# Kernel optimization log

Measured on AMD Instinct MI355X. Metric: run time of the kernel, lower is better.

## Reference

```python
import jax, jax.numpy as jnp
import numpy as np

B = 16384          # batch
NS = 26            # sparse features
ND = 13            # dense features
V = 100000         # vocab per sparse feature
E = 16             # embedding size
H = 400            # dnn hidden
DNN_IN = NS * E + ND  # 429


def setup_inputs() -> dict:
    key = jax.random.key(0)
    ks = jax.random.split(key, 12)
    X_sparse = jax.random.randint(ks[0], (B, NS), 0, V, dtype=jnp.int32)
    X_dense = jax.random.normal(ks[1], (B, ND), dtype=jnp.float32)
    # stacked per-feature embedding tables: [NS, V, dim]
    emb1 = jax.random.normal(ks[2], (NS, V, 1), dtype=jnp.float32) * 1e-4
    emb2 = jax.random.normal(ks[3], (NS, V, E), dtype=jnp.float32) * 1e-4
    lin_weight = jax.random.normal(ks[4], (ND, 1), dtype=jnp.float32) * 1e-4
    bias = jnp.zeros((1,), dtype=jnp.float32)
    W0 = jax.random.normal(ks[5], (DNN_IN, H), dtype=jnp.float32) * 1e-4
    b0 = jnp.zeros((H,), dtype=jnp.float32)
    W1 = jax.random.normal(ks[6], (H, H), dtype=jnp.float32) * 1e-4
    b1 = jnp.zeros((H,), dtype=jnp.float32)
    W2 = jax.random.normal(ks[7], (H, H), dtype=jnp.float32) * 1e-4
    b2 = jnp.zeros((H,), dtype=jnp.float32)
    W_out = jax.random.normal(ks[8], (H, 1), dtype=jnp.float32) * 1e-4
    return {"X_sparse": X_sparse, "X_dense": X_dense, "emb1": emb1, "emb2": emb2,
            "lin_weight": lin_weight, "bias": bias, "W0": W0, "b0": b0,
            "W1": W1, "b1": b1, "W2": W2, "b2": b2, "W_out": W_out}


def reference(X_sparse, X_dense, emb1, emb2, lin_weight, bias, W0, b0, W1, b1, W2, b2, W_out):
    fidx = jnp.arange(NS)[None, :]            # [1, NS] feature indices
    # ---- FM linear term ----
    e1 = emb1[fidx, X_sparse][..., 0]          # [B, NS] per-feature scalar embeddings
    linear_sparse = jnp.sum(e1, axis=-1, keepdims=True)            # [B, 1]
    linear_dense = X_dense @ lin_weight                            # [B, 1]
    logit = linear_sparse + linear_dense
    # ---- FM second-order cross term ----
    e2 = emb2[fidx, X_sparse]                  # [B, NS, E]
    square_of_sum = jnp.square(jnp.sum(e2, axis=1))                # [B, E]
    sum_of_square = jnp.sum(jnp.square(e2), axis=1)                # [B, E]
    cross = 0.5 * jnp.sum(square_of_sum - sum_of_square, axis=-1, keepdims=True)
    logit = logit + cross
    # ---- DNN (dropout p=0 -> identity) ----
    dnn_in = jnp.concatenate([e2.reshape(e2.shape[0], -1), X_dense], axis=-1)  # [B, 429]
    h = jax.nn.relu(dnn_in @ W0 + b0)
    h = jax.nn.relu(h @ W1 + b1)
    h = jax.nn.relu(h @ W2 + b2)
    logit = logit + h @ W_out
    return logit + bias
```

## Files before the change

kernel.cpp:

```cpp
#include <hip/hip_runtime.h>
#include <hip/hip_bf16.h>

#define B_     16384
#define NS_    26
#define ND_    13
#define V_     100000
#define E_     16
#define H_     400
#define NP     448
#define K0A    429

typedef __bf16 bf16x8 __attribute__((ext_vector_type(8)));
typedef float  f32x4  __attribute__((ext_vector_type(4)));

__device__ __forceinline__ unsigned short f2bf(float f) {
  __hip_bfloat16 h = __float2bfloat16(f);
  return __builtin_bit_cast(unsigned short, h);
}

__global__ __launch_bounds__(256) void fm_kernel(
    const int* __restrict__ Xs, const float* __restrict__ Xd,
    const float* __restrict__ emb1, const float* __restrict__ emb2,
    const float* __restrict__ linw, const float* __restrict__ bias,
    unsigned short* __restrict__ dnn, float* __restrict__ out) {
  const int row  = blockIdx.x * 16 + (threadIdx.x >> 4);
  const int lane = threadIdx.x & 15;
  const int* xs = Xs + row * NS_;
  unsigned short* drow = dnn + (size_t)row * NP;

  float s_sum = 0.f, s_sq = 0.f;
#pragma unroll
  for (int f = 0; f < NS_; ++f) {
    int idx = xs[f];
    float v = emb2[((size_t)f * V_ + idx) * E_ + lane];
    s_sum += v;
    s_sq  += v * v;
    drow[f * 16 + lane] = f2bf(v);
  }

  float lin = 0.f;
  for (int f = lane; f < NS_; f += 16)
    lin += emb1[(size_t)f * V_ + xs[f]];

  float xdv = 0.f;
  if (lane < ND_) {
    xdv = Xd[row * ND_ + lane];
    lin += xdv * linw[lane];
  }
  drow[416 + lane] = f2bf(lane < ND_ ? xdv : 0.f);
  drow[432 + lane] = 0;

  float r = 0.5f * (s_sum * s_sum - s_sq) + lin;
#pragma unroll
  for (int m = 8; m >= 1; m >>= 1) r += __shfl_xor(r, m, 64);
  if (lane == 0) out[row] = r + bias[0];
}

__global__ __launch_bounds__(256) void conv_all(
    const float* __restrict__ W0, const float* __restrict__ W1,
    const float* __restrict__ W2, const float* __restrict__ b0,
    const float* __restrict__ b1, const float* __restrict__ b2,
    const float* __restrict__ Wout,
    unsigned short* __restrict__ W0t, unsigned short* __restrict__ W1t,
    unsigned short* __restrict__ W2t, float* __restrict__ b0p,
    float* __restrict__ b1p, float* __restrict__ b2p,
    float* __restrict__ woutp) {
  const int WSZ = NP * NP;
  int i = blockIdx.x * 256 + threadIdx.x;
  if (i < 3 * WSZ) {
    int which = i / WSZ;
    int j = i - which * WSZ;
    int k = j / NP, n = j - (j / NP) * NP;
    const float* W = (which == 0) ? W0 : (which == 1) ? W1 : W2;
    unsigned short* Wt = (which == 0) ? W0t : (which == 1) ? W1t : W2t;
    int Kact = (which == 0) ? K0A : H_;
    float v = (k < Kact && n < H_) ? W[k * H_ + n] : 0.f;
    Wt[(size_t)n * NP + k] = f2bf(v);
  } else {
    int j = i - 3 * WSZ;
    if (j < NP)          b0p[j]            = (j < H_) ? b0[j] : 0.f;
    else if (j < 2 * NP) b1p[j - NP]       = (j - NP < H_) ? b1[j - NP] : 0.f;
    else if (j < 3 * NP) b2p[j - 2 * NP]   = (j - 2 * NP < H_) ? b2[j - 2 * NP] : 0.f;
    else if (j < 4 * NP) woutp[j - 3 * NP] = (j - 3 * NP < H_) ? Wout[j - 3 * NP] : 0.f;
  }
}

__global__ __launch_bounds__(256) void gemm_relu(
    const unsigned short* __restrict__ A, const unsigned short* __restrict__ Bt,
    const float* __restrict__ bias, unsigned short* __restrict__ C,
    const float* __restrict__ wout, float* __restrict__ out, int fuse) {
  __shared__ unsigned short As[128][40];
  __shared__ unsigned short Bs[64][40];

  const int tid  = threadIdx.x;
  const int wave = tid >> 6;
  const int lane = tid & 63;
  const int quad = lane >> 4;
  const int l16  = lane & 15;
  const int rowBase = blockIdx.x * 128;
  const int colBase = blockIdx.y * 64;

  const int sr = tid >> 2, sseg = tid & 3;
  const unsigned short* aptr0 = A  + (size_t)(rowBase + sr) * NP + sseg * 8;
  const unsigned short* aptr1 = A  + (size_t)(rowBase + 64 + sr) * NP + sseg * 8;
  const unsigned short* bptr  = Bt + (size_t)(colBase + sr) * NP + sseg * 8;

  f32x4 acc[2][4] = {};

  uint4 a0 = *(const uint4*)(aptr0);
  uint4 a1 = *(const uint4*)(aptr1);
  uint4 bv = *(const uint4*)(bptr);

  const int nK = NP / 32;
  for (int kt = 0; kt < nK; ++kt) {
    __syncthreads();
    *(uint4*)&As[sr][sseg * 8]      = a0;
    *(uint4*)&As[64 + sr][sseg * 8] = a1;
    *(uint4*)&Bs[sr][sseg * 8]      = bv;
    __syncthreads();

    if (kt + 1 < nK) {
      a0 = *(const uint4*)(aptr0 + (kt + 1) * 32);
      a1 = *(const uint4*)(aptr1 + (kt + 1) * 32);
      bv = *(const uint4*)(bptr + (kt + 1) * 32);
    }

    bf16x8 af0 = __builtin_bit_cast(bf16x8, *(const uint4*)&As[wave * 32 + l16][quad * 8]);
    bf16x8 af1 = __builtin_bit_cast(bf16x8, *(const uint4*)&As[wave * 32 + 16 + l16][quad * 8]);
#pragma unroll
    for (int nt = 0; nt < 4; ++nt) {
      bf16x8 bf = __builtin_bit_cast(bf16x8, *(const uint4*)&Bs[nt * 16 + l16][quad * 8]);
      acc[0][nt] = __builtin_amdgcn_mfma_f32_16x16x32_bf16(af0, bf, acc[0][nt], 0, 0, 0);
      acc[1][nt] = __builtin_amdgcn_mfma_f32_16x16x32_bf16(af1, bf, acc[1][nt], 0, 0, 0);
    }
  }

  float wsum[2][4] = {};
#pragma unroll
  for (int mt = 0; mt < 2; ++mt) {
#pragma unroll
    for (int nt = 0; nt < 4; ++nt) {
      int col = colBase + nt * 16 + l16;
      float bz = bias[col];
      float wv = wout[col];
#pragma unroll
      for (int r = 0; r < 4; ++r) {
        float v = acc[mt][nt][r] + bz;
        v = v > 0.f ? v : 0.f;
        if (!fuse) {
          int row = rowBase + wave * 32 + mt * 16 + quad * 4 + r;
          C[(size_t)row * NP + col] = f2bf(v);
        } else {
          wsum[mt][r] += v * wv;
        }
      }
    }
  }

  if (fuse) {
#pragma unroll
    for (int mt = 0; mt < 2; ++mt) {
#pragma unroll
      for (int r = 0; r < 4; ++r) {
        float s = wsum[mt][r];
        s += __shfl_xor(s, 1, 64);
        s += __shfl_xor(s, 2, 64);
        s += __shfl_xor(s, 4, 64);
        s += __shfl_xor(s, 8, 64);
        if (l16 == 0) {
          int row = rowBase + wave * 32 + mt * 16 + quad * 4 + r;
          atomicAdd(out + row, s);
        }
      }
    }
  }
}

extern "C" void kernel_launch(void* const* d_in, const int* in_sizes, int n_in,
                              void* d_out, int out_size, void* d_ws, size_t ws_size,
                              hipStream_t stream) {
  const int*   Xs   = (const int*)d_in[0];
  const float* Xd   = (const float*)d_in[1];
  const float* emb1 = (const float*)d_in[2];
  const float* emb2 = (const float*)d_in[3];
  const float* linw = (const float*)d_in[4];
  const float* bias = (const float*)d_in[5];
  const float* W0   = (const float*)d_in[6];
  const float* b0   = (const float*)d_in[7];
  const float* W1   = (const float*)d_in[8];
  const float* b1   = (const float*)d_in[9];
  const float* W2   = (const float*)d_in[10];
  const float* b2   = (const float*)d_in[11];
  const float* Wout = (const float*)d_in[12];
  float* out = (float*)d_out;

  char* ws = (char*)d_ws;
  const size_t PSZ = (size_t)B_ * NP * 2;
  const size_t WSZ = (size_t)NP * NP * 2;
  unsigned short* P0  = (unsigned short*)(ws);
  unsigned short* P1  = (unsigned short*)(ws + PSZ);
  unsigned short* W0t = (unsigned short*)(ws + 2 * PSZ);
  unsigned short* W1t = (unsigned short*)(ws + 2 * PSZ + WSZ);
  unsigned short* W2t = (unsigned short*)(ws + 2 * PSZ + 2 * WSZ);
  float* b0p   = (float*)(ws + 2 * PSZ + 3 * WSZ);
  float* b1p   = (float*)(ws + 2 * PSZ + 3 * WSZ + 1792);
  float* b2p   = (float*)(ws + 2 * PSZ + 3 * WSZ + 2 * 1792);
  float* woutp = (float*)(ws + 2 * PSZ + 3 * WSZ + 3 * 1792);

  fm_kernel<<<B_ / 16, 256, 0, stream>>>(Xs, Xd, emb1, emb2, linw, bias, P0, out);

  conv_all<<<(3 * NP * NP + 4 * NP) / 256, 256, 0, stream>>>(
      W0, W1, W2, b0, b1, b2, Wout, W0t, W1t, W2t, b0p, b1p, b2p, woutp);

  dim3 grid(B_ / 128, NP / 64);
  gemm_relu<<<grid, 256, 0, stream>>>(P0, W0t, b0p, P1, woutp, out, 0);
  gemm_relu<<<grid, 256, 0, stream>>>(P1, W1t, b1p, P0, woutp, out, 0);
  gemm_relu<<<grid, 256, 0, stream>>>(P0, W2t, b2p, P1, woutp, out, 1);
}
```

Baseline: 297.0 us.

## Fuse three DNN layers into one kernel keeping activations in LDS

Replaces the three separate GEMM launches with one kernel per 64-row tile. The tile's activations stay in shared memory across all three layers, and weight K-chunks are streamed through a double buffer with async global-to-LDS loads. The embedding gather and the weight conversion are merged into a single prep launch, and the conversion indexing is changed to write coalesced. This removes the global round-trips of the intermediate activations and two launches, but it re-streams all weights for every tile and runs at one block per CU because of the large LDS footprint.

```diff
diff --git a/kernel.cpp b/kernel.cpp
--- a/kernel.cpp
+++ b/kernel.cpp
@@ -5,10 +5,13 @@
 #define NS_    26
 #define ND_    13
 #define V_     100000
-#define E_     16
 #define H_     400
 #define NP     448
 #define K0A    429
+#define MT     64
+#define ASTR   456
+#define WCH    (448 * 32)
+#define LDSB   (MT * ASTR * 2 + 2 * WCH * 2)
 
 typedef __bf16 bf16x8 __attribute__((ext_vector_type(8)));
 typedef float  f32x4  __attribute__((ext_vector_type(4)));
@@ -18,158 +21,189 @@
   return __builtin_bit_cast(unsigned short, h);
 }
 
-__global__ __launch_bounds__(256) void fm_kernel(
+__global__ __launch_bounds__(256) void prep_kernel(
     const int* __restrict__ Xs, const float* __restrict__ Xd,
     const float* __restrict__ emb1, const float* __restrict__ emb2,
     const float* __restrict__ linw, const float* __restrict__ bias,
-    unsigned short* __restrict__ dnn, float* __restrict__ out) {
-  const int row  = blockIdx.x * 16 + (threadIdx.x >> 4);
-  const int lane = threadIdx.x & 15;
-  const int* xs = Xs + row * NS_;
-  unsigned short* drow = dnn + (size_t)row * NP;
-
-  float s_sum = 0.f, s_sq = 0.f;
-#pragma unroll
-  for (int f = 0; f < NS_; ++f) {
-    int idx = xs[f];
-    float v = emb2[((size_t)f * V_ + idx) * E_ + lane];
-    s_sum += v;
-    s_sq  += v * v;
-    drow[f * 16 + lane] = f2bf(v);
-  }
-
-  float lin = 0.f;
-  for (int f = lane; f < NS_; f += 16)
-    lin += emb1[(size_t)f * V_ + xs[f]];
-
-  float xdv = 0.f;
-  if (lane < ND_) {
-    xdv = Xd[row * ND_ + lane];
-    lin += xdv * linw[lane];
-  }
-  drow[416 + lane] = f2bf(lane < ND_ ? xdv : 0.f);
-  drow[432 + lane] = 0;
-
-  float r = 0.5f * (s_sum * s_sum - s_sq) + lin;
-#pragma unroll
-  for (int m = 8; m >= 1; m >>= 1) r += __shfl_xor(r, m, 64);
-  if (lane == 0) out[row] = r + bias[0];
-}
-
-__global__ __launch_bounds__(256) void conv_all(
     const float* __restrict__ W0, const float* __restrict__ W1,
     const float* __restrict__ W2, const float* __restrict__ b0,
     const float* __restrict__ b1, const float* __restrict__ b2,
     const float* __restrict__ Wout,
-    unsigned short* __restrict__ W0t, unsigned short* __restrict__ W1t,
-    unsigned short* __restrict__ W2t, float* __restrict__ b0p,
-    float* __restrict__ b1p, float* __restrict__ b2p,
-    float* __restrict__ woutp) {
-  const int WSZ = NP * NP;
-  int i = blockIdx.x * 256 + threadIdx.x;
-  if (i < 3 * WSZ) {
-    int which = i / WSZ;
-    int j = i - which * WSZ;
-    int k = j / NP, n = j - (j / NP) * NP;
-    const float* W = (which == 0) ? W0 : (which == 1) ? W1 : W2;
-    unsigned short* Wt = (which == 0) ? W0t : (which == 1) ? W1t : W2t;
-    int Kact = (which == 0) ? K0A : H_;
-    float v = (k < Kact && n < H_) ? W[k * H_ + n] : 0.f;
-    Wt[(size_t)n * NP + k] = f2bf(v);
+    unsigned short* __restrict__ dnn, unsigned short* __restrict__ W0t,
+    unsigned short* __restrict__ W1t, unsigned short* __restrict__ W2t,
+    float* __restrict__ b0p, float* __restrict__ b1p, float* __restrict__ b2p,
+    float* __restrict__ woutp, float* __restrict__ out) {
+  const int blk = blockIdx.x;
+  if (blk < 1024) {
+    const int row  = blk * 16 + (threadIdx.x >> 4);
+    const int lane = threadIdx.x & 15;
+    const int* xs = Xs + row * NS_;
+    unsigned short* drow = dnn + (size_t)row * NP;
+
+    float s_sum = 0.f, s_sq = 0.f;
+#pragma unroll
+    for (int f = 0; f < NS_; ++f) {
+      int idx = xs[f];
+      float v = emb2[((size_t)f * V_ + idx) * 16 + lane];
+      s_sum += v;
+      s_sq  += v * v;
+      drow[f * 16 + lane] = f2bf(v);
+    }
+    float lin = 0.f;
+    for (int f = lane; f < NS_; f += 16)
+      lin += emb1[(size_t)f * V_ + xs[f]];
+    float xdv = 0.f;
+    if (lane < ND_) {
+      xdv = Xd[row * ND_ + lane];
+      lin += xdv * linw[lane];
+    }
+    drow[416 + lane] = f2bf(lane < ND_ ? xdv : 0.f);
+    drow[432 + lane] = 0;
+
+    float r = 0.5f * (s_sum * s_sum - s_sq) + lin;
+#pragma unroll
+    for (int m = 8; m >= 1; m >>= 1) r += __shfl_xor(r, m, 64);
+    if (lane == 0) out[row] = r + bias[0];
   } else {
-    int j = i - 3 * WSZ;
-    if (j < NP)          b0p[j]            = (j < H_) ? b0[j] : 0.f;
-    else if (j < 2 * NP) b1p[j - NP]       = (j - NP < H_) ? b1[j - NP] : 0.f;
-    else if (j < 3 * NP) b2p[j - 2 * NP]   = (j - 2 * NP < H_) ? b2[j - 2 * NP] : 0.f;
-    else if (j < 4 * NP) woutp[j - 3 * NP] = (j - 3 * NP < H_) ? Wout[j - 3 * NP] : 0.f;
-  }
-}
-
-__global__ __launch_bounds__(256) void gemm_relu(
-    const unsigned short* __restrict__ A, const unsigned short* __restrict__ Bt,
-    const float* __restrict__ bias, unsigned short* __restrict__ C,
-    const float* __restrict__ wout, float* __restrict__ out, int fuse) {
-  __shared__ unsigned short As[128][40];
-  __shared__ unsigned short Bs[64][40];
+    const int WSZ = NP * NP;
+    int i = (blk - 1024) * 256 + threadIdx.x;
+    if (i < 3 * WSZ) {
+      int which = i / WSZ;
+      int j = i - which * WSZ;
+      int n = j / NP, k = j - (j / NP) * NP;
+      const float* W = (which == 0) ? W0 : (which == 1) ? W1 : W2;
+      unsigned short* Wt = (which == 0) ? W0t : (which == 1) ? W1t : W2t;
+      int Kact = (which == 0) ? K0A : H_;
+      float v = (k < Kact && n < H_) ? W[k * H_ + n] : 0.f;
+      Wt[(size_t)n * NP + k] = f2bf(v);
+    } else {
+      int j = i - 3 * WSZ;
+      if (j < NP)          b0p[j]            = (j < H_) ? b0[j] : 0.f;
+      else if (j < 2 * NP) b1p[j - NP]       = (j - NP < H_) ? b1[j - NP] : 0.f;
+      else if (j < 3 * NP) b2p[j - 2 * NP]   = (j - 2 * NP < H_) ? b2[j - 2 * NP] : 0.f;
+      else if (j < 4 * NP) woutp[j - 3 * NP] = (j - 3 * NP < H_) ? Wout[j - 3 * NP] : 0.f;
+    }
+  }
+}
+
+__device__ __forceinline__ void stage_w_chunk(
+    const unsigned short* __restrict__ Wt, int kt, unsigned short* wb,
+    int wave, int lane) {
+#pragma unroll
+  for (int i = 0; i < 7; ++i) {
+    int sbase = i * 256 + wave * 64;
+    int s = sbase + lane;
+    int n = s >> 2, g = s & 3;
+    const unsigned short* gp = Wt + n * NP + kt * 32 + g * 8;
+    unsigned short* lp = wb + (size_t)sbase * 8;
+    __builtin_amdgcn_global_load_lds(
+        (const __attribute__((address_space(1))) unsigned int*)gp,
+        (__attribute__((address_space(3))) unsigned int*)lp, 16, 0, 0);
+  }
+}
+
+__global__ __launch_bounds__(256, 1) void fused_dnn(
+    const unsigned short* __restrict__ dnn,
+    const unsigned short* __restrict__ W0t, const unsigned short* __restrict__ W1t,
+    const unsigned short* __restrict__ W2t,
+    const float* __restrict__ b0p, const float* __restrict__ b1p,
+    const float* __restrict__ b2p, const float* __restrict__ woutp,
+    float* __restrict__ out) {
+  extern __shared__ char smem[];
+  unsigned short* act  = (unsigned short*)smem;
+  unsigned short* wbuf = (unsigned short*)(smem + MT * ASTR * 2);
 
   const int tid  = threadIdx.x;
   const int wave = tid >> 6;
   const int lane = tid & 63;
   const int quad = lane >> 4;
   const int l16  = lane & 15;
-  const int rowBase = blockIdx.x * 128;
-  const int colBase = blockIdx.y * 64;
-
-  const int sr = tid >> 2, sseg = tid & 3;
-  const unsigned short* aptr0 = A  + (size_t)(rowBase + sr) * NP + sseg * 8;
-  const unsigned short* aptr1 = A  + (size_t)(rowBase + 64 + sr) * NP + sseg * 8;
-  const unsigned short* bptr  = Bt + (size_t)(colBase + sr) * NP + sseg * 8;
-
-  f32x4 acc[2][4] = {};
-
-  uint4 a0 = *(const uint4*)(aptr0);
-  uint4 a1 = *(const uint4*)(aptr1);
-  uint4 bv = *(const uint4*)(bptr);
-
-  const int nK = NP / 32;
-  for (int kt = 0; kt < nK; ++kt) {
+  const int r0   = blockIdx.x * MT;
+
+#pragma unroll
+  for (int i = 0; i < 7; ++i) {
+    int s = i * 256 + tid;
+    int row = s / 28, gc = s - (s / 28) * 28;
+    uint4 v = *(const uint4*)(dnn + (size_t)(r0 + row) * NP + gc * 8);
+    *(uint4*)(act + row * ASTR + gc * 8) = v;
+  }
+
+  const unsigned short* Wl[3] = {W0t, W1t, W2t};
+  const float* bl[3] = {b0p, b1p, b2p};
+
+  stage_w_chunk(Wl[0], 0, wbuf, wave, lane);
+
+  for (int layer = 0; layer < 3; ++layer) {
+    const unsigned short* Wt = Wl[layer];
+    f32x4 acc[4][7] = {};
+
+    for (int kt = 0; kt < 14; ++kt) {
+      __syncthreads();
+      if (kt + 1 < 14)
+        stage_w_chunk(Wt, kt + 1, wbuf + ((kt + 1) & 1) * WCH, wave, lane);
+      const unsigned short* wb = wbuf + (kt & 1) * WCH;
+
+      bf16x8 af[4];
+#pragma unroll
+      for (int mt = 0; mt < 4; ++mt)
+        af[mt] = __builtin_bit_cast(
+            bf16x8, *(const uint4*)(act + (mt * 16 + l16) * ASTR + kt * 32 + quad * 8));
+#pragma unroll
+      for (int nt = 0; nt < 7; ++nt) {
+        int n = wave * 112 + nt * 16 + l16;
+        bf16x8 bf = __builtin_bit_cast(bf16x8, *(const uint4*)(wb + n * 32 + quad * 8));
+#pragma unroll
+        for (int mt = 0; mt < 4; ++mt)
+          acc[mt][nt] = __builtin_amdgcn_mfma_f32_16x16x32_bf16(af[mt], bf, acc[mt][nt], 0, 0, 0);
+      }
+    }
+
     __syncthreads();
-    *(uint4*)&As[sr][sseg * 8]      = a0;
-    *(uint4*)&As[64 + sr][sseg * 8] = a1;
-    *(uint4*)&Bs[sr][sseg * 8]      = bv;
-    __syncthreads();
-
-    if (kt + 1 < nK) {
-      a0 = *(const uint4*)(aptr0 + (kt + 1) * 32);
-      a1 = *(const uint4*)(aptr1 + (kt + 1) * 32);
-      bv = *(const uint4*)(bptr + (kt + 1) * 32);
-    }
-
-    bf16x8 af0 = __builtin_bit_cast(bf16x8, *(const uint4*)&As[wave * 32 + l16][quad * 8]);
-    bf16x8 af1 = __builtin_bit_cast(bf16x8, *(const uint4*)&As[wave * 32 + 16 + l16][quad * 8]);
-#pragma unroll
-    for (int nt = 0; nt < 4; ++nt) {
-      bf16x8 bf = __builtin_bit_cast(bf16x8, *(const uint4*)&Bs[nt * 16 + l16][quad * 8]);
-      acc[0][nt] = __builtin_amdgcn_mfma_f32_16x16x32_bf16(af0, bf, acc[0][nt], 0, 0, 0);
-      acc[1][nt] = __builtin_amdgcn_mfma_f32_16x16x32_bf16(af1, bf, acc[1][nt], 0, 0, 0);
-    }
-  }
-
-  float wsum[2][4] = {};
-#pragma unroll
-  for (int mt = 0; mt < 2; ++mt) {
-#pragma unroll
-    for (int nt = 0; nt < 4; ++nt) {
-      int col = colBase + nt * 16 + l16;
-      float bz = bias[col];
-      float wv = wout[col];
-#pragma unroll
-      for (int r = 0; r < 4; ++r) {
-        float v = acc[mt][nt][r] + bz;
-        v = v > 0.f ? v : 0.f;
-        if (!fuse) {
-          int row = rowBase + wave * 32 + mt * 16 + quad * 4 + r;
-          C[(size_t)row * NP + col] = f2bf(v);
-        } else {
-          wsum[mt][r] += v * wv;
+
+    if (layer < 2) {
+      stage_w_chunk(Wl[layer + 1], 0, wbuf, wave, lane);
+#pragma unroll
+      for (int nt = 0; nt < 7; ++nt) {
+        int col = wave * 112 + nt * 16 + l16;
+        float bz = bl[layer][col];
+#pragma unroll
+        for (int mt = 0; mt < 4; ++mt) {
+#pragma unroll
+          for (int r = 0; r < 4; ++r) {
+            float v = acc[mt][nt][r] + bz;
+            v = v > 0.f ? v : 0.f;
+            act[(mt * 16 + quad * 4 + r) * ASTR + col] = f2bf(v);
+          }
         }
       }
-    }
-  }
-
-  if (fuse) {
-#pragma unroll
-    for (int mt = 0; mt < 2; ++mt) {
-#pragma unroll
-      for (int r = 0; r < 4; ++r) {
-        float s = wsum[mt][r];
-        s += __shfl_xor(s, 1, 64);
-        s += __shfl_xor(s, 2, 64);
-        s += __shfl_xor(s, 4, 64);
-        s += __shfl_xor(s, 8, 64);
-        if (l16 == 0) {
-          int row = rowBase + wave * 32 + mt * 16 + quad * 4 + r;
-          atomicAdd(out + row, s);
+    } else {
+      float wsum[4][4] = {};
+#pragma unroll
+      for (int nt = 0; nt < 7; ++nt) {
+        int col = wave * 112 + nt * 16 + l16;
+        float bz = bl[2][col];
+        float wv = woutp[col];
+#pragma unroll
+        for (int mt = 0; mt < 4; ++mt) {
+#pragma unroll
+          for (int r = 0; r < 4; ++r) {
+            float v = acc[mt][nt][r] + bz;
+            v = v > 0.f ? v : 0.f;
+            wsum[mt][r] += v * wv;
+          }
+        }
+      }
+#pragma unroll
+      for (int mt = 0; mt < 4; ++mt) {
+#pragma unroll
+        for (int r = 0; r < 4; ++r) {
+          float s = wsum[mt][r];
+          s += __shfl_xor(s, 1, 64);
+          s += __shfl_xor(s, 2, 64);
+          s += __shfl_xor(s, 4, 64);
+          s += __shfl_xor(s, 8, 64);
+          if (l16 == 0)
+            atomicAdd(out + r0 + mt * 16 + quad * 4 + r, s);
         }
       }
     }
@@ -198,22 +232,21 @@
   const size_t PSZ = (size_t)B_ * NP * 2;
   const size_t WSZ = (size_t)NP * NP * 2;
   unsigned short* P0  = (unsigned short*)(ws);
-  unsigned short* P1  = (unsigned short*)(ws + PSZ);
-  unsigned short* W0t = (unsigned short*)(ws + 2 * PSZ);
-  unsigned short* W1t = (unsigned short*)(ws + 2 * PSZ + WSZ);
-  unsigned short* W2t = (unsigned short*)(ws + 2 * PSZ + 2 * WSZ);
-  float* b0p   = (float*)(ws + 2 * PSZ + 3 * WSZ);
-  float* b1p   = (float*)(ws + 2 * PSZ + 3 * WSZ + 1792);
-  float* b2p   = (float*)(ws + 2 * PSZ + 3 * WSZ + 2 * 1792);
-  float* woutp = (float*)(ws + 2 * PSZ + 3 * WSZ + 3 * 1792);
-
-  fm_kernel<<<B_ / 16, 256, 0, stream>>>(Xs, Xd, emb1, emb2, linw, bias, P0, out);
-
-  conv_all<<<(3 * NP * NP + 4 * NP) / 256, 256, 0, stream>>>(
-      W0, W1, W2, b0, b1, b2, Wout, W0t, W1t, W2t, b0p, b1p, b2p, woutp);
-
-  dim3 grid(B_ / 128, NP / 64);
-  gemm_relu<<<grid, 256, 0, stream>>>(P0, W0t, b0p, P1, woutp, out, 0);
-  gemm_relu<<<grid, 256, 0, stream>>>(P1, W1t, b1p, P0, woutp, out, 0);
-  gemm_relu<<<grid, 256, 0, stream>>>(P0, W2t, b2p, P1, woutp, out, 1);
-}
+  unsigned short* W0t = (unsigned short*)(ws + PSZ);
+  unsigned short* W1t = (unsigned short*)(ws + PSZ + WSZ);
+  unsigned short* W2t = (unsigned short*)(ws + PSZ + 2 * WSZ);
+  float* b0p   = (float*)(ws + PSZ + 3 * WSZ);
+  float* b1p   = (float*)(ws + PSZ + 3 * WSZ + 1792);
+  float* b2p   = (float*)(ws + PSZ + 3 * WSZ + 2 * 1792);
+  float* woutp = (float*)(ws + PSZ + 3 * WSZ + 3 * 1792);
+
+  (void)hipFuncSetAttribute((const void*)fused_dnn,
+                            hipFuncAttributeMaxDynamicSharedMemorySize, LDSB);
+
+  prep_kernel<<<1024 + 2359, 256, 0, stream>>>(
+      Xs, Xd, emb1, emb2, linw, bias, W0, W1, W2, b0, b1, b2, Wout,
+      P0, W0t, W1t, W2t, b0p, b1p, b2p, woutp, out);
+
+  fused_dnn<<<B_ / MT, 256, LDSB, stream>>>(
+      P0, W0t, W1t, W2t, b0p, b1p, b2p, woutp, out);
+}
```

New measurement: 284.5 us. 1.04x faster.
